# Kernel tuning notes

Measured on AMD Instinct MI355X. Metric: run time of the kernel, lower is better.

## Reference

```python
import jax, jax.numpy as jnp
import numpy as np

D_MODEL = 1024
NUM_HEADS = 16
HEAD_DIM = D_MODEL // NUM_HEADS
THETA = 10000.0
BATCH = 2
SEQ = 2048


def _apply_rope(x, positions):
    # x: (b, h, s, hd), positions: (b, s) int
    hd = x.shape[-1]
    inv_freq = 1.0 / (THETA ** (jnp.arange(0, hd, 2, dtype=jnp.float32) / hd))  # (hd/2,)
    ang = positions.astype(jnp.float32)[:, None, :, None] * inv_freq  # (b,1,s,hd/2)
    cos, sin = jnp.cos(ang), jnp.sin(ang)
    x1 = x[..., 0::2]
    x2 = x[..., 1::2]
    r1 = x1 * cos - x2 * sin
    r2 = x1 * sin + x2 * cos
    return jnp.stack([r1, r2], axis=-1).reshape(x.shape)


def setup_inputs() -> dict:
    key = jax.random.key(0)
    ks = jax.random.split(key, 5)
    scale = 1.0 / np.sqrt(D_MODEL)
    x = jax.random.normal(ks[0], (BATCH, SEQ, D_MODEL), dtype=jnp.float32)
    token_positions = jnp.broadcast_to(jnp.arange(SEQ, dtype=jnp.int32), (BATCH, SEQ))
    W_q = jax.random.normal(ks[1], (D_MODEL, D_MODEL), dtype=jnp.float32) * scale
    W_k = jax.random.normal(ks[2], (D_MODEL, D_MODEL), dtype=jnp.float32) * scale
    W_v = jax.random.normal(ks[3], (D_MODEL, D_MODEL), dtype=jnp.float32) * scale
    W_o = jax.random.normal(ks[4], (D_MODEL, D_MODEL), dtype=jnp.float32) * scale
    return {"x": x, "token_positions": token_positions, "W_q": W_q, "W_k": W_k, "W_v": W_v, "W_o": W_o}


def reference(x, token_positions, W_q, W_k, W_v, W_o):
    b, s, _ = x.shape
    h, hd = NUM_HEADS, HEAD_DIM
    # bias-free Linear: y = x @ W^T, W: (out, in)
    def proj(W):
        return jnp.einsum('bsd,ed->bse', x, W).reshape(b, s, h, hd).transpose(0, 2, 1, 3)
    Q = _apply_rope(proj(W_q), token_positions)
    K = _apply_rope(proj(W_k), token_positions)
    V = proj(W_v)
    scores = jnp.einsum('bhqd,bhkd->bhqk', Q, K) / jnp.sqrt(jnp.float32(hd))
    causal = jnp.triu(jnp.full((s, s), -jnp.inf, dtype=scores.dtype), k=1)
    attn = jax.nn.softmax(scores + causal, axis=-1)
    Z = jnp.einsum('bhqk,bhkd->bhqd', attn, V)
    Z = Z.transpose(0, 2, 1, 3).reshape(b, s, h * hd)
    return jnp.einsum('bse,de->bsd', Z, W_o)
```

## Files before the change

### kernel.cpp

```cpp
#include <hip/hip_runtime.h>
#include <hip/hip_bf16.h>


#define BATCH 2
#define SEQ   2048
#define NH    16
#define HD    64
#define DM    1024
#define MTOT  (BATCH*SEQ)

typedef __attribute__((ext_vector_type(8))) short bf16x8;
typedef __attribute__((ext_vector_type(4))) float f32x4;
typedef __attribute__((ext_vector_type(4))) unsigned int u32x4;
typedef unsigned short u16;
typedef unsigned int   u32;

__device__ __forceinline__ float b2f(u16 h){ return __uint_as_float(((u32)h) << 16); }
__device__ __forceinline__ u16 f2b(float f){
  u32 u = __float_as_uint(f);
  u32 r = (u + 0x7FFFu + ((u >> 16) & 1u)) >> 16;
  return (u16)r;
}
__device__ __forceinline__ u16 cvt1(float f){
  __hip_bfloat16 h = __float2bfloat16(f);
  return *reinterpret_cast<u16*>(&h);
}
__device__ __forceinline__ u32 pk2(float lo, float hi){
  return (u32)cvt1(lo) | ((u32)cvt1(hi) << 16);
}
__device__ __forceinline__ f32x4 mfma16(bf16x8 a, bf16x8 b, f32x4 c){
  return __builtin_amdgcn_mfma_f32_16x16x32_bf16(a, b, c, 0, 0, 0);
}
__device__ __forceinline__ void gload_lds16(const u16* g, u16* l){
  __builtin_amdgcn_global_load_lds((const __attribute__((address_space(1))) unsigned int*)g,
                                   (__attribute__((address_space(3))) unsigned int*)l, 16, 0, 0);
}

__global__ __launch_bounds__(256) void cvt_all(const float* __restrict__ x,
    const float* __restrict__ wq, const float* __restrict__ wk,
    const float* __restrict__ wv, const float* __restrict__ wo,
    u16* __restrict__ xb, u16* __restrict__ wb)
{
  const long NX = (long)MTOT * DM;
  const long NW = (long)DM * DM;
  const long tot4 = (NX + 4*NW) >> 2;
  for (long t = (long)blockIdx.x*blockDim.x + threadIdx.x; t < tot4;
       t += (long)gridDim.x*blockDim.x){
    long e = t << 2;
    const float* s; u16* d;
    if (e < NX){ s = x + e; d = xb + e; }
    else {
      long j = e - NX; int z = (int)(j >> 20);
      const float* ws = (z==0)?wq:(z==1)?wk:(z==2)?wv:wo;
      s = ws + (j & (NW-1)); d = wb + j;
    }
    float4 v = *(const float4*)s;
    u32 lo = (u32)f2b(v.x) | ((u32)f2b(v.y) << 16);
    u32 hi = (u32)f2b(v.z) | ((u32)f2b(v.w) << 16);
    uint2 o; o.x = lo; o.y = hi;
    *(uint2*)d = o;
  }
}

__global__ __launch_bounds__(256) void rope_table(float2* __restrict__ tab){
  int t = blockIdx.x*blockDim.x + threadIdx.x;
  if (t >= SEQ*32) return;
  int s = t >> 5, i = t & 31;
  float inv = 1.0f / powf(10000.0f, (float)i * (1.0f/32.0f));
  float a = (float)s * inv;
  tab[t] = make_float2(cosf(a), sinf(a));
}

__global__ __launch_bounds__(256) void gemm_qkv(const u16* __restrict__ xb,
                                                const u16* __restrict__ wb,
                                                u16* __restrict__ Qd, u16* __restrict__ Kd,
                                                u16* __restrict__ Vt,
                                                const float2* __restrict__ tab,
                                                const int* __restrict__ pos)
{
  __shared__ u16 Alds[128*64];
  __shared__ u16 Blds[64*64];
  const int fid = blockIdx.x;
  const int xj = fid & 7, tt = fid >> 3;
  const int mb = (tt/48)*8 + xj;
  const int rest = tt % 48;
  const int nb = rest & 15, z = rest >> 4;
  const u16* Bm = wb + (long)z * DM * DM;
  const int nbase = nb*64, mbase = mb*128;
  const int tid = threadIdx.x;
  const int w = tid >> 6, l = tid & 63, g = l >> 4, c = l & 15;
  const int wr = (w >> 1)*64, wc = (w & 1)*32;
  const int srow = l >> 3;
  const int scol = ((l & 7) ^ srow)*8;
  const u16* Ag = xb + (long)(mbase + w*32 + srow)*DM + scol;
  const u16* Bg = Bm + (long)(nbase + w*16 + srow)*DM + scol;
  u16* Alb = Alds + w*2048;
  u16* Blb = Blds + w*1024;
  f32x4 acc[4][2] = {};

  for (int k0 = 0; k0 < DM; k0 += 64){
    __syncthreads();
    #pragma unroll
    for (int i = 0; i < 4; i++)
      gload_lds16(Ag + k0 + (long)(8*i)*DM, Alb + i*512);
    #pragma unroll
    for (int i = 0; i < 2; i++)
      gload_lds16(Bg + k0 + (long)(8*i)*DM, Blb + i*512);
    __syncthreads();
    #pragma unroll
    for (int ks = 0; ks < 2; ks++){
      bf16x8 af[4], bfr[2];
      #pragma unroll
      for (int mi = 0; mi < 4; mi++){
        int row = wr + mi*16 + c;
        af[mi] = *(const bf16x8*)&Alds[row*64 + (((ks*4 + g) ^ (row & 7))*8)];
      }
      #pragma unroll
      for (int nj = 0; nj < 2; nj++){
        int row = wc + nj*16 + c;
        bfr[nj] = *(const bf16x8*)&Blds[row*64 + (((ks*4 + g) ^ (row & 7))*8)];
      }
      #pragma unroll
      for (int mi = 0; mi < 4; mi++)
        #pragma unroll
        for (int nj = 0; nj < 2; nj++)
          acc[mi][nj] = mfma16(af[mi], bfr[nj], acc[mi][nj]);
    }
  }

  if (z == 2){
    #pragma unroll
    for (int mi = 0; mi < 4; mi++){
      int row0 = mbase + wr + mi*16 + 4*g;
      int bb = row0 >> 11, s0 = row0 & (SEQ-1);
      #pragma unroll
      for (int nj = 0; nj < 2; nj++){
        int col = nbase + wc + nj*16 + c;
        int hh = col >> 6, d = col & 63;
        ushort4 v;
        v.x = cvt1(acc[mi][nj][0]); v.y = cvt1(acc[mi][nj][1]);
        v.z = cvt1(acc[mi][nj][2]); v.w = cvt1(acc[mi][nj][3]);
        *(ushort4*)&Vt[((long)(bb*NH + hh)*HD + d)*SEQ + s0] = v;
      }
    }
  } else {
    u16* Out = (z == 0) ? Qd : Kd;
    const float scale = (z == 0) ? 0.125f*1.44269504089f : 1.f;
    const bool even = (c & 1) == 0;
    #pragma unroll
    for (int mi = 0; mi < 4; mi++){
      #pragma unroll
      for (int r = 0; r < 4; r++){
        int row = mbase + wr + mi*16 + 4*g + r;
        int bb = row >> 11, s = row & (SEQ-1);
        int p = pos[bb*SEQ + s];
        if (p < 0) p = 0; if (p >= SEQ) p = SEQ - 1;
        #pragma unroll
        for (int nj = 0; nj < 2; nj++){
          int col = nbase + wc + nj*16 + c;
          float2 cs = tab[p*32 + ((col & 63) >> 1)];
          float own = acc[mi][nj][r];
          float prt = __shfl_xor(own, 1);
          float rr = even ? (own*cs.x - prt*cs.y) : (prt*cs.y + own*cs.x);
          rr *= scale;
          Out[(long)row*DM + col] = cvt1(rr);
        }
      }
    }
  }
}

__global__ __launch_bounds__(256) void gemm_out(const u16* __restrict__ Zb,
                                                const u16* __restrict__ wob,
                                                float* __restrict__ out)
{
  __shared__ u16 Alds[128*64];
  __shared__ u16 Blds[64*64];
  const int fid = blockIdx.x;
  const int xj = fid & 7, tt = fid >> 3;
  const int mb = (tt/16)*8 + xj;
  const int nb = tt % 16;
  const int nbase = nb*64, mbase = mb*128;
  const int tid = threadIdx.x;
  const int w = tid >> 6, l = tid & 63, g = l >> 4, c = l & 15;
  const int wr = (w >> 1)*64, wc = (w & 1)*32;
  const int srow = l >> 3;
  const int scol = ((l & 7) ^ srow)*8;
  const u16* Ag = Zb  + (long)(mbase + w*32 + srow)*DM + scol;
  const u16* Bg = wob + (long)(nbase + w*16 + srow)*DM + scol;
  u16* Alb = Alds + w*2048;
  u16* Blb = Blds + w*1024;
  f32x4 acc[4][2] = {};

  for (int k0 = 0; k0 < DM; k0 += 64){
    __syncthreads();
    #pragma unroll
    for (int i = 0; i < 4; i++)
      gload_lds16(Ag + k0 + (long)(8*i)*DM, Alb + i*512);
    #pragma unroll
    for (int i = 0; i < 2; i++)
      gload_lds16(Bg + k0 + (long)(8*i)*DM, Blb + i*512);
    __syncthreads();
    #pragma unroll
    for (int ks = 0; ks < 2; ks++){
      bf16x8 af[4], bfr[2];
      #pragma unroll
      for (int mi = 0; mi < 4; mi++){
        int row = wr + mi*16 + c;
        af[mi] = *(const bf16x8*)&Alds[row*64 + (((ks*4 + g) ^ (row & 7))*8)];
      }
      #pragma unroll
      for (int nj = 0; nj < 2; nj++){
        int row = wc + nj*16 + c;
        bfr[nj] = *(const bf16x8*)&Blds[row*64 + (((ks*4 + g) ^ (row & 7))*8)];
      }
      #pragma unroll
      for (int mi = 0; mi < 4; mi++)
        #pragma unroll
        for (int nj = 0; nj < 2; nj++)
          acc[mi][nj] = mfma16(af[mi], bfr[nj], acc[mi][nj]);
    }
  }
  #pragma unroll
  for (int mi = 0; mi < 4; mi++)
    #pragma unroll
    for (int nj = 0; nj < 2; nj++)
      #pragma unroll
      for (int r = 0; r < 4; r++){
        int row = mbase + wr + mi*16 + 4*g + r;
        int col = nbase + wc + nj*16 + c;
        out[(long)row*DM + col] = acc[mi][nj][r];
      }
}

__device__ __forceinline__ int kperm(int a){
  return (a & 32) | ((a & 4) << 2) | ((a & 24) >> 1) | (a & 3);
}

__global__ __launch_bounds__(256) void attn(const u16* __restrict__ Q, const u16* __restrict__ K,
                                            const u16* __restrict__ Vt,
                                            u16* __restrict__ Opart, float* __restrict__ Lsum)
{
  const int fid = blockIdx.x;
  const int xj = fid & 7, tt = fid >> 3;
  const int grp = (tt >> 5)*8 + xj;
  const int within = tt & 31;
  const int h = grp & 15, b = grp >> 4;
  const int pair = within >> 1;
  const int half = within & 1;
  const int tid = threadIdx.x, w = tid >> 6, l = tid & 63, g = l >> 4, c = l & 15;
  const u16* Kp = K  + (long)(b*SEQ)*DM + h*HD;
  const u16* Vp = Vt + (long)(b*NH + h)*HD*SEQ;

  __shared__ u16 KV[2][2][64][64];
  u16* kv = &KV[0][0][0][0];

  const int srow0 = tid >> 3, sch = tid & 7;
  const int kpr0 = kperm(srow0), kpr1 = kperm(srow0 + 32);
  const int cswz = c & 7;

  const int wk0 = kpr0*64 + (sch ^ (kpr0 & 7))*8;
  const int wk1 = kpr1*64 + (sch ^ (kpr1 & 7))*8;
  const int wv0 = 4096 + srow0*64 + (sch ^ (srow0 & 7))*8;
  const int wv1 = 4096 + (srow0 + 32)*64 + (sch ^ ((srow0 + 32) & 7))*8;
  const int ra0 = c*64 + (((0 + g) ^ cswz)*8);
  const int ra1 = c*64 + (((4 + g) ^ cswz)*8);

  bf16x8 ones;
  #pragma unroll
  for (int j = 0; j < 8; j++) ones[j] = (short)0x3F80;

  int bufo = 0;
  #pragma unroll 1
  for (int seg = 0; seg < 2; ++seg){
    const int qt = seg ? (31 - pair) : pair;
    const int qbase = qt*64;
    const int qrow = qbase + w*16;
    const u16* Qp = Q + (long)(b*SEQ + qrow)*DM + h*HD;
    bf16x8 qf0 = *(const bf16x8*)(Qp + c*DM + g*8);
    bf16x8 qf1 = *(const bf16x8*)(Qp + c*DM + 32 + g*8);

    const int ntH0  = (qt + 2) >> 1;
    const int tstart = half ? ntH0 : 0;
    const int tend   = half ? (qt + 1) : ntH0;

    f32x4 accz[4] = {};
    f32x4 lacc = {};

    if (tstart < tend){
      __syncthreads();
      const u16* kg0 = Kp + (long)(tstart*64 + srow0)*DM + sch*8;
      const u16* kg1 = kg0 + (long)32*DM;
      const u16* vg0 = Vp + (long)srow0*SEQ + tstart*64 + sch*8;
      const u16* vg1 = vg0 + 32*SEQ;
      bf16x8 kr0 = *(const bf16x8*)kg0, kr1 = *(const bf16x8*)kg1;
      bf16x8 vr0 = *(const bf16x8*)vg0, vr1 = *(const bf16x8*)vg1;
      kg0 += (long)64*DM; kg1 += (long)64*DM; vg0 += 64; vg1 += 64;
      *(bf16x8*)(kv + bufo + wk0) = kr0;
      *(bf16x8*)(kv + bufo + wk1) = kr1;
      *(bf16x8*)(kv + bufo + wv0) = vr0;
      *(bf16x8*)(kv + bufo + wv1) = vr1;

      for (int t = tstart; t < tend; ++t){
        const int kbase = t*64;
        __syncthreads();

        if (t < tend-1){
          kr0 = *(const bf16x8*)kg0; kr1 = *(const bf16x8*)kg1;
          vr0 = *(const bf16x8*)vg0; vr1 = *(const bf16x8*)vg1;
          kg0 += (long)64*DM; kg1 += (long)64*DM; vg0 += 64; vg1 += 64;
        }

        const u16* kvb = kv + bufo;

        f32x4 s[4];
        __builtin_amdgcn_s_setprio(1);
        #pragma unroll
        for (int sub = 0; sub < 4; sub++){
          bf16x8 ka0 = *(const bf16x8*)(kvb + ra0 + sub*1024);
          bf16x8 ka1 = *(const bf16x8*)(kvb + ra1 + sub*1024);
          f32x4 z4 = {};
          z4 = mfma16(ka0, qf0, z4);
          z4 = mfma16(ka1, qf1, z4);
          s[sub] = z4;
        }
        __builtin_amdgcn_s_setprio(0);

        const bool edge = (kbase + 63 > qrow);
        const int q = qrow + c;
        if (edge){
          #pragma unroll
          for (int sub = 0; sub < 4; sub++)
            #pragma unroll
            for (int r = 0; r < 4; r++){
              int key = kbase + ((sub >> 1) << 5) + 8*g + ((sub & 1) << 2) + r;
              if (key > q) s[sub][r] = -1e30f;
            }
        }
        #pragma unroll
        for (int sub = 0; sub < 4; sub++)
          #pragma unroll
          for (int r = 0; r < 4; r++)
            s[sub][r] = exp2f(s[sub][r]);

        u32x4 p0, p1;
        p0[0] = pk2(s[0][0], s[0][1]); p0[1] = pk2(s[0][2], s[0][3]);
        p0[2] = pk2(s[1][0], s[1][1]); p0[3] = pk2(s[1][2], s[1][3]);
        p1[0] = pk2(s[2][0], s[2][1]); p1[1] = pk2(s[2][2], s[2][3]);
        p1[2] = pk2(s[3][0], s[3][1]); p1[3] = pk2(s[3][2], s[3][3]);
        bf16x8 pf0 = __builtin_bit_cast(bf16x8, p0);
        bf16x8 pf1 = __builtin_bit_cast(bf16x8, p1);

        __builtin_amdgcn_s_setprio(1);
        lacc = mfma16(pf0, ones, lacc);
        lacc = mfma16(pf1, ones, lacc);
        #pragma unroll
        for (int dt = 0; dt < 4; dt++){
          bf16x8 vf0 = *(const bf16x8*)(kvb + 4096 + ra0 + dt*1024);
          bf16x8 vf1 = *(const bf16x8*)(kvb + 4096 + ra1 + dt*1024);
          accz[dt] = mfma16(pf0, vf0, accz[dt]);
          accz[dt] = mfma16(pf1, vf1, accz[dt]);
        }
        __builtin_amdgcn_s_setprio(0);

        if (t < tend-1){
          int nbo = bufo ^ 8192;
          *(bf16x8*)(kv + nbo + wk0) = kr0;
          *(bf16x8*)(kv + nbo + wk1) = kr1;
          *(bf16x8*)(kv + nbo + wv0) = vr0;
          *(bf16x8*)(kv + nbo + wv1) = vr1;
          bufo = nbo;
        }
      }
    }

    const int pbase = (((b*NH + h)*32 + qt)*2 + half);
    if (c == 0){
      #pragma unroll
      for (int r = 0; r < 4; r++)
        Lsum[pbase*64 + w*16 + 4*g + r] = lacc[r];
    }
    u16* Op = Opart + (long)pbase*(64*64);
    #pragma unroll
    for (int dt = 0; dt < 4; dt++)
      #pragma unroll
      for (int r = 0; r < 4; r++)
        Op[(w*16 + 4*g + r)*64 + dt*16 + c] = cvt1(accz[dt][r]);
  }
}

__global__ __launch_bounds__(256) void attn_combine(const u16* __restrict__ Opart,
                                                    const float* __restrict__ Lsum,
                                                    u16* __restrict__ Z)
{
  const int qt = blockIdx.x, h = blockIdx.y, b = blockIdx.z;
  const int p0 = ((b*NH + h)*32 + qt)*2, p1 = p0 + 1;
  const int row = threadIdx.x >> 2;
  const int d0  = (threadIdx.x & 3)*16;
  float inv = 1.f / (Lsum[p0*64 + row] + Lsum[p1*64 + row]);
  const u16* o0 = Opart + ((long)p0*64 + row)*64 + d0;
  const u16* o1 = Opart + ((long)p1*64 + row)*64 + d0;
  const int s = qt*64 + row;
  u16* zp = Z + (long)(b*SEQ + s)*DM + h*HD + d0;
  #pragma unroll
  for (int j = 0; j < 2; j++){
    bf16x8 va = *(const bf16x8*)(o0 + j*8);
    bf16x8 vb = *(const bf16x8*)(o1 + j*8);
    bf16x8 ov;
    #pragma unroll
    for (int e = 0; e < 8; e++){
      float z = (b2f((u16)va[e]) + b2f((u16)vb[e]))*inv;
      ov[e] = (short)cvt1(z);
    }
    *(bf16x8*)(zp + j*8) = ov;
  }
}

extern "C" void kernel_launch(void* const* d_in, const int* in_sizes, int n_in,
                              void* d_out, int out_size, void* d_ws, size_t ws_size,
                              hipStream_t stream)
{
  const float* x  = (const float*)d_in[0];
  const int*   pos= (const int*)d_in[1];
  const float* wq = (const float*)d_in[2];
  const float* wk = (const float*)d_in[3];
  const float* wv = (const float*)d_in[4];
  const float* wo = (const float*)d_in[5];
  float* out = (float*)d_out;

  const long NX = (long)MTOT*DM;
  const long NW = (long)DM*DM;
  char* p = (char*)d_ws;
  u16* xb   = (u16*)p;  p += NX*2;
  u16* wb   = (u16*)p;  p += 4*NW*2;
  u16* Qd   = (u16*)p;  p += NX*2;
  u16* Kd   = (u16*)p;  p += NX*2;
  u16* Vt   = (u16*)p;  p += NX*2;
  u16* Zb   = (u16*)p;  p += NX*2;
  float2* tab = (float2*)p; p += (long)SEQ*32*sizeof(float2);
  u16* Opart = (u16*)p;  p += 2L*NX*2;
  float* Lsum = (float*)p; p += 2048L*64*sizeof(float);
  (void)ws_size; (void)n_in; (void)in_sizes; (void)out_size;

  hipLaunchKernelGGL(cvt_all,     dim3(2048),      dim3(256), 0, stream, x, wq, wk, wv, wo, xb, wb);
  hipLaunchKernelGGL(rope_table,  dim3(256),       dim3(256), 0, stream, tab);
  hipLaunchKernelGGL(gemm_qkv,    dim3(1536),      dim3(256), 0, stream, xb, wb, Qd, Kd, Vt, tab, pos);
  hipLaunchKernelGGL(attn,        dim3(1024),      dim3(256), 0, stream, Qd, Kd, Vt, Opart, Lsum);
  hipLaunchKernelGGL(attn_combine,dim3(32,16,2),   dim3(256), 0, stream, Opart, Lsum, Zb);
  hipLaunchKernelGGL(gemm_out,    dim3(512),       dim3(256), 0, stream, Zb, wb + 3*NW, out);
}
```

Before: 116.7 us.

## Load K/V tiles directly into LDS with global_load_lds instead of register staging

Replaces the register-staged global-to-LDS copy of K and V tiles in the attention kernel with direct global-to-LDS loads (gload_lds16). The swizzle and permutation move from the LDS write address to the global read address (an inverse permutation), so each wave writes a contiguous LDS region. This frees VGPRs and removes the separate ds_write step after compute. The trade-off is reliance on correct waitcnt and barrier ordering for the async LDS writes, and possibly less coalesced global reads.

```diff
diff --git a/kernel.cpp b/kernel.cpp
--- a/kernel.cpp
+++ b/kernel.cpp
@@ -233,8 +233,8 @@
       }
 }
 
-__device__ __forceinline__ int kperm(int a){
-  return (a & 32) | ((a & 4) << 2) | ((a & 24) >> 1) | (a & 3);
+__device__ __forceinline__ int kinv(int s){
+  return (s & 32) | ((s & 16) >> 2) | ((s & 12) << 1) | (s & 3);
 }
 
 __global__ __launch_bounds__(256) void attn(const u16* __restrict__ Q, const u16* __restrict__ K,
@@ -255,14 +255,15 @@
   __shared__ u16 KV[2][2][64][64];
   u16* kv = &KV[0][0][0][0];
 
-  const int srow0 = tid >> 3, sch = tid & 7;
-  const int kpr0 = kperm(srow0), kpr1 = kperm(srow0 + 32);
+  const int lrow0 = w*8 + (l >> 3), lrow1 = lrow0 + 32, lch = l & 7;
+  const long ks0 = (long)kinv(lrow0)*DM + ((lch ^ (lrow0 & 7))*8);
+  const long ks1 = (long)kinv(lrow1)*DM + ((lch ^ (lrow1 & 7))*8);
+  const long vs0 = (long)lrow0*SEQ + ((lch ^ (lrow0 & 7))*8);
+  const long vs1 = (long)lrow1*SEQ + ((lch ^ (lrow1 & 7))*8);
+  const int kd0 = w*512, kd1 = kd0 + 2048;
+  const int vd0 = 4096 + kd0, vd1 = 4096 + kd1;
+
   const int cswz = c & 7;
-
-  const int wk0 = kpr0*64 + (sch ^ (kpr0 & 7))*8;
-  const int wk1 = kpr1*64 + (sch ^ (kpr1 & 7))*8;
-  const int wv0 = 4096 + srow0*64 + (sch ^ (srow0 & 7))*8;
-  const int wv1 = 4096 + (srow0 + 32)*64 + (sch ^ ((srow0 + 32) & 7))*8;
   const int ra0 = c*64 + (((0 + g) ^ cswz)*8);
   const int ra1 = c*64 + (((4 + g) ^ cswz)*8);
 
@@ -289,26 +290,25 @@
 
     if (tstart < tend){
       __syncthreads();
-      const u16* kg0 = Kp + (long)(tstart*64 + srow0)*DM + sch*8;
-      const u16* kg1 = kg0 + (long)32*DM;
-      const u16* vg0 = Vp + (long)srow0*SEQ + tstart*64 + sch*8;
-      const u16* vg1 = vg0 + 32*SEQ;
-      bf16x8 kr0 = *(const bf16x8*)kg0, kr1 = *(const bf16x8*)kg1;
-      bf16x8 vr0 = *(const bf16x8*)vg0, vr1 = *(const bf16x8*)vg1;
-      kg0 += (long)64*DM; kg1 += (long)64*DM; vg0 += 64; vg1 += 64;
-      *(bf16x8*)(kv + bufo + wk0) = kr0;
-      *(bf16x8*)(kv + bufo + wk1) = kr1;
-      *(bf16x8*)(kv + bufo + wv0) = vr0;
-      *(bf16x8*)(kv + bufo + wv1) = vr1;
+      const u16* kgp = Kp + (long)(tstart*64)*DM;
+      const u16* vgp = Vp + tstart*64;
+      gload_lds16(kgp + ks0, kv + bufo + kd0);
+      gload_lds16(kgp + ks1, kv + bufo + kd1);
+      gload_lds16(vgp + vs0, kv + bufo + vd0);
+      gload_lds16(vgp + vs1, kv + bufo + vd1);
+      kgp += (long)64*DM; vgp += 64;
 
       for (int t = tstart; t < tend; ++t){
         const int kbase = t*64;
         __syncthreads();
 
         if (t < tend-1){
-          kr0 = *(const bf16x8*)kg0; kr1 = *(const bf16x8*)kg1;
-          vr0 = *(const bf16x8*)vg0; vr1 = *(const bf16x8*)vg1;
-          kg0 += (long)64*DM; kg1 += (long)64*DM; vg0 += 64; vg1 += 64;
+          int nbo = bufo ^ 8192;
+          gload_lds16(kgp + ks0, kv + nbo + kd0);
+          gload_lds16(kgp + ks1, kv + nbo + kd1);
+          gload_lds16(vgp + vs0, kv + nbo + vd0);
+          gload_lds16(vgp + vs1, kv + nbo + vd1);
+          kgp += (long)64*DM; vgp += 64;
         }
 
         const u16* kvb = kv + bufo;
@@ -363,14 +363,7 @@
         }
         __builtin_amdgcn_s_setprio(0);
 
-        if (t < tend-1){
-          int nbo = bufo ^ 8192;
-          *(bf16x8*)(kv + nbo + wk0) = kr0;
-          *(bf16x8*)(kv + nbo + wk1) = kr1;
-          *(bf16x8*)(kv + nbo + wv0) = vr0;
-          *(bf16x8*)(kv + nbo + wv1) = vr1;
-          bufo = nbo;
-        }
+        if (t < tend-1) bufo ^= 8192;
       }
     }
 
```

Measured after the change: 117.2 us, median of 2. Within noise of the previous version (+0.4%).
